# Kernel tuning notes

Measured on AMD Instinct MI355X. Metric: run time of the kernel, lower is better.

Reference implementation:

```python
import jax, jax.numpy as jnp
import numpy as np

NUM_HEADS = 16


def setup_inputs() -> dict:
    key = jax.random.key(0)
    k1, k2, k3 = jax.random.split(key, 3)
    B, N, C = 4, 2048, 1024
    x = jax.random.normal(k1, (B, N, C), dtype=jnp.float32)
    qkv_w = jax.random.normal(k2, (3 * C, C), dtype=jnp.float32) * (C ** -0.5)
    proj_w = jax.random.normal(k3, (C, C), dtype=jnp.float32) * (C ** -0.5)
    proj_b = jnp.zeros((C,), dtype=jnp.float32)
    return {"x": x, "qkv_w": qkv_w, "proj_w": proj_w, "proj_b": proj_b, "len_t": 256}


def reference(x, qkv_w, proj_w, proj_b, len_t):
    B, N, C = x.shape
    H = NUM_HEADS
    hd = C // H
    scale = hd ** -0.5
    # qkv: [B, N, 3C] -> [3, B, H, N, hd]
    qkv = (x @ qkv_w.T).reshape(B, N, 3, H, hd).transpose(2, 0, 3, 1, 4)
    q, k, v = qkv[0], qkv[1], qkv[2]
    q_s = q[:, :, len_t:]                      # [B, H, N-len_t, hd] partial queries
    attn = jnp.einsum('bhqd,bhkd->bhqk', q_s, k) * scale
    attn = jax.nn.softmax(attn, axis=-1)       # [B, H, N-len_t, N]
    x_s = jnp.einsum('bhqk,bhkd->bhqd', attn, v)
    x_s = x_s.transpose(0, 2, 1, 3).reshape(B, N - len_t, C)
    x_t = x[:, :len_t]                         # template tokens pass through
    x_out = jnp.concatenate((x_t, x_s), axis=1)
    return x_out @ proj_w.T + proj_b
```

## Files before the change

kernel.cpp:

```cpp
#include <hip/hip_runtime.h>
#include <stdint.h>

typedef unsigned short u16;
typedef __attribute__((ext_vector_type(4))) short short4v;
typedef __attribute__((ext_vector_type(8))) short short8;
typedef __attribute__((ext_vector_type(4))) float floatx4;
typedef __attribute__((ext_vector_type(4))) unsigned short u16x4;

typedef __attribute__((address_space(1))) const void* gas_ptr;
typedef __attribute__((address_space(3))) void* las_ptr;

__device__ __forceinline__ void async16(const void* g, void* l) {
    __builtin_amdgcn_global_load_lds((gas_ptr)g, (las_ptr)l, 16, 0, 0);
}

__device__ __forceinline__ u16 f2bf(float f) {
    union { float f; unsigned int u; } v; v.f = f;
    unsigned int r = v.u + 0x7fffu + ((v.u >> 16) & 1u);
    return (u16)(r >> 16);
}

__device__ __forceinline__ int pk_bf16(float a, float b) {
    return (int)((unsigned int)f2bf(a) | ((unsigned int)f2bf(b) << 16));
}

__device__ __forceinline__ int pk2t(float a, float b) {
    union { float f; unsigned int u; } ua, ub;
    ua.f = a; ub.f = b;
    return (int)__builtin_amdgcn_perm(ub.u, ua.u, 0x07060302u);
}

__global__ void cvt_w_kernel(const float* __restrict__ src, u16* __restrict__ dst) {
    int i = blockIdx.x * 256 + threadIdx.x;
    float4 f = reinterpret_cast<const float4*>(src)[i];
    u16x4 o;
    o.x = f2bf(f.x); o.y = f2bf(f.y); o.z = f2bf(f.z); o.w = f2bf(f.w);
    reinterpret_cast<u16x4*>(dst)[i] = o;
}

__global__ void cvt_x_kernel(const float* __restrict__ x, u16* __restrict__ xb,
                             u16* __restrict__ xout) {
    int i = blockIdx.x * 256 + threadIdx.x;
    float4 f = reinterpret_cast<const float4*>(x)[i];
    u16x4 o;
    o.x = f2bf(f.x); o.y = f2bf(f.y); o.z = f2bf(f.z); o.w = f2bf(f.w);
    reinterpret_cast<u16x4*>(xb)[i] = o;
    int m = (i * 4) >> 10;
    if ((m & 2047) < 256) reinterpret_cast<u16x4*>(xout)[i] = o;
}

template<int MODE>
__global__ void __launch_bounds__(256, 2)
gemm_nt(const u16* __restrict__ A, const u16* __restrict__ B,
        u16* __restrict__ q_out, u16* __restrict__ k_out, u16* __restrict__ vt_out,
        float* __restrict__ f_out, const float* __restrict__ bias, int K) {
    __shared__ u16 As[128 * 32];
    __shared__ u16 Bs[128 * 32];
    const int tid  = threadIdx.x;
    const int lane = tid & 63;
    const int w    = tid >> 6;
    const int row0 = blockIdx.x * 128;
    const int col0 = blockIdx.y * 128;
    const int wm   = (w >> 1) * 64;
    const int wn   = (w & 1) * 64;

    floatx4 acc[4][4] = {};

    for (int k0 = 0; k0 < K; k0 += 32) {
        __syncthreads();
#pragma unroll
        for (int i = 0; i < 2; ++i) {
            int pb = w * 128 + i * 64;
            int p  = pb + lane;
            int r  = p >> 2;
            int c  = (p & 3) ^ ((r >> 1) & 3);
            async16(A + (size_t)(row0 + r) * K + (k0 + c * 8), (char*)As + pb * 16);
            async16(B + (size_t)(col0 + r) * K + (k0 + c * 8), (char*)Bs + pb * 16);
        }
        __syncthreads();

        short8 af[4], bf_[4];
#pragma unroll
        for (int t = 0; t < 4; ++t) {
            int ar = wm + t * 16 + (lane & 15);
            int ca = (lane >> 4) ^ ((ar >> 1) & 3);
            af[t]  = *(const short8*)(As + ar * 32 + ca * 8);
            int br = wn + t * 16 + (lane & 15);
            int cb = (lane >> 4) ^ ((br >> 1) & 3);
            bf_[t] = *(const short8*)(Bs + br * 32 + cb * 8);
        }
#pragma unroll
        for (int i = 0; i < 4; ++i)
#pragma unroll
            for (int j = 0; j < 4; ++j)
                acc[i][j] = __builtin_amdgcn_mfma_f32_16x16x32_bf16(af[i], bf_[j], acc[i][j], 0, 0, 0);
    }

#pragma unroll
    for (int i = 0; i < 4; ++i) {
#pragma unroll
        for (int j = 0; j < 4; ++j) {
            int gr0 = row0 + wm + i * 16 + ((lane >> 4) << 2);
            int gc  = col0 + wn + j * 16 + (lane & 15);
            if (MODE == 0) {
                int which = gc >> 10;
                int cl = gc & 1023;
                int h = cl >> 6, d = cl & 63;
                int b = gr0 >> 11, n0 = gr0 & 2047;
                int bh = b * 16 + h;
                if (which == 2) {
                    u16x4 pk;
                    pk.x = f2bf(acc[i][j][0]); pk.y = f2bf(acc[i][j][1]);
                    pk.z = f2bf(acc[i][j][2]); pk.w = f2bf(acc[i][j][3]);
                    size_t off = (size_t)bh * 131072
                               + (((size_t)(n0 >> 5) * 4 + (d >> 4)) * 64
                                  + ((n0 >> 3) & 3) * 16 + (d & 15)) * 8 + (n0 & 4);
                    *reinterpret_cast<u16x4*>(vt_out + off) = pk;
                } else {
                    u16* dst = (which == 0) ? q_out : k_out;
                    float sc = (which == 0) ? 0.18033688f : 1.0f;
#pragma unroll
                    for (int r = 0; r < 4; ++r)
                        dst[((size_t)bh * 2048 + n0 + r) * 64 + d] = f2bf(acc[i][j][r] * sc);
                }
            } else {
                float bv = bias[gc];
#pragma unroll
                for (int r = 0; r < 4; ++r)
                    f_out[(size_t)(gr0 + r) * 1024 + gc] = acc[i][j][r] + bv;
            }
        }
    }
}

__global__ void __launch_bounds__(256, 3)
flash_attn(const u16* __restrict__ Qg, const u16* __restrict__ Kg,
           const u16* __restrict__ Vf, u16* __restrict__ xout) {
    __shared__ u16 Ks[2][64 * 64];
    const int lane = threadIdx.x & 63;
    const int w    = threadIdx.x >> 6;
    const int bh   = blockIdx.x & 63;
    const int qt   = blockIdx.x >> 6;
    const int q0   = 256 + qt * 128 + w * 32;
    const size_t kvbase = (size_t)bh * 2048 * 64;

    const int m = lane & 15;
    const int g = lane >> 4;

    short8 qf[2][2];
#pragma unroll
    for (int qs = 0; qs < 2; ++qs) {
        const u16* p = Qg + kvbase + (size_t)(q0 + qs * 16 + m) * 64 + g * 8;
        qf[qs][0] = *(const short8*)(p);
        qf[qs][1] = *(const short8*)(p + 32);
    }

    const u16* vp = Vf + (size_t)bh * 131072 + lane * 8;

    const int p0 = w * 64 + lane;
#define STAGE_K(buf, kt)                                                        \
    {                                                                           \
        _Pragma("unroll")                                                       \
        for (int i = 0; i < 2; ++i) {                                           \
            int p = i * 256 + p0;                                               \
            int r = p >> 3;                                                     \
            int c = (p & 7) ^ ((((r >> 3) & 1) << 2) | (r & 3));                \
            async16(Kg + kvbase + (size_t)((kt) * 64 + r) * 64 + c * 8,         \
                    (char*)&Ks[buf][0] + p * 16);                               \
        }                                                                       \
    }

    STAGE_K(0, 0);

    const floatx4 ZROW = {-32.f, -32.f, -32.f, -32.f};
    short8 ones1;
#pragma unroll
    for (int i = 0; i < 8; ++i) ones1[i] = (short)0x3F80;

    floatx4 lacc[2] = {};
    floatx4 o[2][4] = {};

    const int fm = ((m >> 2) & 1) * 4 + (m & 3);

    for (int kt = 0; kt < 32; ++kt) {
        __syncthreads();
        if (kt + 1 < 32) STAGE_K((kt + 1) & 1, kt + 1);

        const u16* kbuf = &Ks[kt & 1][0];
#pragma unroll
        for (int b32 = 0; b32 < 2; ++b32) {
            short8 vfr[4];
#pragma unroll
            for (int i = 0; i < 4; ++i)
                vfr[i] = *(const short8*)(vp + (size_t)((kt * 2 + b32) * 4 + i) * 512);

            floatx4 sT[2][2];
#pragma unroll
            for (int t = 0; t < 2; ++t) {
                int r = b32 * 32 + (m >> 2) * 8 + t * 4 + (m & 3);
                short8 k0 = *(const short8*)(kbuf + r * 64 + ((g)     ^ fm) * 8);
                short8 k1 = *(const short8*)(kbuf + r * 64 + ((4 + g) ^ fm) * 8);
                __builtin_amdgcn_s_setprio(1);
#pragma unroll
                for (int qs = 0; qs < 2; ++qs) {
                    floatx4 z = __builtin_amdgcn_mfma_f32_16x16x32_bf16(k0, qf[qs][0], ZROW, 0, 0, 0);
                    sT[qs][t] = __builtin_amdgcn_mfma_f32_16x16x32_bf16(k1, qf[qs][1], z, 0, 0, 0);
                }
                __builtin_amdgcn_s_setprio(0);
            }

#pragma unroll
            for (int qs = 0; qs < 2; ++qs) {
                float p[8];
#pragma unroll
                for (int t = 0; t < 2; ++t)
#pragma unroll
                    for (int r = 0; r < 4; ++r)
                        p[t * 4 + r] = __builtin_amdgcn_exp2f(sT[qs][t][r]);
                union { int i4[4]; short8 s8; } u;
                u.i4[0] = pk2t(p[0], p[1]);
                u.i4[1] = pk2t(p[2], p[3]);
                u.i4[2] = pk2t(p[4], p[5]);
                u.i4[3] = pk2t(p[6], p[7]);
                __builtin_amdgcn_s_setprio(1);
#pragma unroll
                for (int i = 0; i < 4; ++i)
                    o[qs][i] = __builtin_amdgcn_mfma_f32_16x16x32_bf16(vfr[i], u.s8, o[qs][i], 0, 0, 0);
                lacc[qs] = __builtin_amdgcn_mfma_f32_16x16x32_bf16(ones1, u.s8, lacc[qs], 0, 0, 0);
                __builtin_amdgcn_s_setprio(0);
            }
        }
    }

    const int b = bh >> 4, h = bh & 15;
#pragma unroll
    for (int qs = 0; qs < 2; ++qs) {
        const float inv = 1.f / lacc[qs][0];

        const int n = q0 + qs * 16 + m;
        u16* dst = xout + (size_t)(b * 2048 + n) * 1024 + h * 64 + (g << 2);
#pragma unroll
        for (int i = 0; i < 4; ++i) {
            union { int i2[2]; u16x4 s4; } u;
            u.i2[0] = pk_bf16(o[qs][i][0] * inv, o[qs][i][1] * inv);
            u.i2[1] = pk_bf16(o[qs][i][2] * inv, o[qs][i][3] * inv);
            *reinterpret_cast<u16x4*>(dst + i * 16) = u.s4;
        }
    }
#undef STAGE_K
}

extern "C" void kernel_launch(void* const* d_in, const int* in_sizes, int n_in,
                              void* d_out, int out_size, void* d_ws, size_t ws_size,
                              hipStream_t stream) {
    const float* x      = (const float*)d_in[0];
    const float* qkv_w  = (const float*)d_in[1];
    const float* proj_w = (const float*)d_in[2];
    const float* proj_b = (const float*)d_in[3];

    char* ws = (char*)d_ws;
    u16* xb    = (u16*)(ws);
    u16* xout  = (u16*)(ws + ((size_t)16 << 20));
    u16* wqkv  = (u16*)(ws + ((size_t)32 << 20));
    u16* wproj = (u16*)(ws + ((size_t)38 << 20));
    u16* Qb    = (u16*)(ws + ((size_t)40 << 20));
    u16* Kb    = (u16*)(ws + ((size_t)56 << 20));
    u16* Vfb   = (u16*)(ws + ((size_t)72 << 20));

    cvt_x_kernel<<<8192, 256, 0, stream>>>(x, xb, xout);
    cvt_w_kernel<<<3072, 256, 0, stream>>>(qkv_w, wqkv);
    cvt_w_kernel<<<1024, 256, 0, stream>>>(proj_w, wproj);
    gemm_nt<0><<<dim3(64, 24), 256, 0, stream>>>(xb, wqkv, Qb, Kb, Vfb, nullptr, nullptr, 1024);
    flash_attn<<<896, 256, 0, stream>>>(Qb, Kb, Vfb, xout);
    gemm_nt<1><<<dim3(64, 8), 256, 0, stream>>>(xout, wproj, nullptr, nullptr, nullptr,
                                                (float*)d_out, proj_b, 1024);
}
```

Before: 250.4 us.

## Double-buffer LDS tiles in the bf16 GEMM to overlap global loads with MFMA

Shared-memory tiles for A and B in the NT GEMM get two buffers. The next K-slice's async global-to-LDS loads are issued before the current slice's MFMAs, and one barrier per iteration replaces two. The aim is to hide global load latency behind matrix math. LDS use doubles. If the compiler inserts a conservative vmcnt wait before the LDS reads, the overlap may not happen.

```diff
diff --git a/kernel.cpp b/kernel.cpp
--- a/kernel.cpp
+++ b/kernel.cpp
@@ -54,8 +54,8 @@
 gemm_nt(const u16* __restrict__ A, const u16* __restrict__ B,
         u16* __restrict__ q_out, u16* __restrict__ k_out, u16* __restrict__ vt_out,
         float* __restrict__ f_out, const float* __restrict__ bias, int K) {
-    __shared__ u16 As[128 * 32];
-    __shared__ u16 Bs[128 * 32];
+    __shared__ u16 As[2][128 * 32];
+    __shared__ u16 Bs[2][128 * 32];
     const int tid  = threadIdx.x;
     const int lane = tid & 63;
     const int w    = tid >> 6;
@@ -66,28 +66,39 @@
 
     floatx4 acc[4][4] = {};
 
-    for (int k0 = 0; k0 < K; k0 += 32) {
+#define STAGE_G(buf, kbyte)                                                     \
+    {                                                                           \
+        _Pragma("unroll")                                                       \
+        for (int i = 0; i < 2; ++i) {                                           \
+            int pb = w * 128 + i * 64;                                          \
+            int p  = pb + lane;                                                 \
+            int r  = p >> 2;                                                    \
+            int c  = (p & 3) ^ ((r >> 1) & 3);                                  \
+            async16(A + (size_t)(row0 + r) * K + ((kbyte) + c * 8),             \
+                    (char*)&As[buf][0] + p * 16);                               \
+            async16(B + (size_t)(col0 + r) * K + ((kbyte) + c * 8),             \
+                    (char*)&Bs[buf][0] + p * 16);                               \
+        }                                                                       \
+    }
+
+    STAGE_G(0, 0);
+    const int nk = K >> 5;
+
+    for (int kt = 0; kt < nk; ++kt) {
         __syncthreads();
-#pragma unroll
-        for (int i = 0; i < 2; ++i) {
-            int pb = w * 128 + i * 64;
-            int p  = pb + lane;
-            int r  = p >> 2;
-            int c  = (p & 3) ^ ((r >> 1) & 3);
-            async16(A + (size_t)(row0 + r) * K + (k0 + c * 8), (char*)As + pb * 16);
-            async16(B + (size_t)(col0 + r) * K + (k0 + c * 8), (char*)Bs + pb * 16);
-        }
-        __syncthreads();
-
+        if (kt + 1 < nk) STAGE_G((kt + 1) & 1, (kt + 1) << 5);
+
+        const u16* as = &As[kt & 1][0];
+        const u16* bs = &Bs[kt & 1][0];
         short8 af[4], bf_[4];
 #pragma unroll
         for (int t = 0; t < 4; ++t) {
             int ar = wm + t * 16 + (lane & 15);
             int ca = (lane >> 4) ^ ((ar >> 1) & 3);
-            af[t]  = *(const short8*)(As + ar * 32 + ca * 8);
+            af[t]  = *(const short8*)(as + ar * 32 + ca * 8);
             int br = wn + t * 16 + (lane & 15);
             int cb = (lane >> 4) ^ ((br >> 1) & 3);
-            bf_[t] = *(const short8*)(Bs + br * 32 + cb * 8);
+            bf_[t] = *(const short8*)(bs + br * 32 + cb * 8);
         }
 #pragma unroll
         for (int i = 0; i < 4; ++i)
@@ -95,6 +106,7 @@
             for (int j = 0; j < 4; ++j)
                 acc[i][j] = __builtin_amdgcn_mfma_f32_16x16x32_bf16(af[i], bf_[j], acc[i][j], 0, 0, 0);
     }
+#undef STAGE_G
 
 #pragma unroll
     for (int i = 0; i < 4; ++i) {
```

Measured after the change: 255.6 us. +2.1%, slower.
